# Kernel optimization log

Measured on AMD Instinct MI355X. Metric: run time of the kernel, lower is better.

The kernel has to match this reference:

```python
import jax, jax.numpy as jnp
import numpy as np

EPS = 1e-6


def setup_inputs() -> dict:
    key = jax.random.key(0)
    k1, k2 = jax.random.split(key)
    B, T = 1048576, 16
    # pred = [mean_x, mean_y, var_x, var_y]; rand keeps variances positive.
    pred = jax.random.uniform(k1, (B, 4), dtype=jnp.float32)
    true = jax.random.normal(k2, (B, T, 2), dtype=jnp.float32)
    return {"pred": pred, "true": true}


def reference(pred, true):
    # true_dist = N(tm, diag(tv)), pred_dist = N(pm, diag(pv)); loss = mean_i KL(true_i || pred_i)
    pm = pred[:, :2]                     # [B,2]
    pv = pred[:, 2:] + EPS               # [B,2]
    tm = jnp.mean(true, axis=1)          # [B,2]
    tv = jnp.var(true, axis=1, ddof=1) + EPS  # unbiased, matching torch .var()
    # Closed-form diagonal-Gaussian KL(p||q) = 0.5 * sum(log(qv/pv) + pv/qv + (qm-pm)^2/qv - 1)
    kl = 0.5 * (jnp.sum(jnp.log(pv / tv) + tv / pv + (pm - tm) ** 2 / pv, axis=-1) - 2.0)
    return jnp.mean(kl)
```

## Files before the change

### kernel.cpp

```cpp
#include <hip/hip_runtime.h>

#define KLD_EPS 1e-6f

__global__ __launch_bounds__(256) void gaze_kld_partial(
    const float* __restrict__ pred,
    const float* __restrict__ tru,
    float* __restrict__ partial,
    int B, int nTiles)
{
    __shared__ float4 lds4[2048];

    const int t    = threadIdx.x;
    const int lane = t & 63;
    const int wid  = t >> 6;

    const float4* __restrict__ tru4  = (const float4*)tru;
    const float4* __restrict__ pred4 = (const float4*)pred;

    float local = 0.0f;
    const long long totF4 = (long long)B * 8;

    for (int tb = blockIdx.x; tb < nTiles; tb += gridDim.x) {
        const long long gBase = (long long)tb * 2048;
        const int row = tb * 256 + t;

        float4 p = make_float4(0.f, 0.f, 1.f, 1.f);
        if (row < B) p = pred4[row];

        if ((tb * 256 + 256) <= B) {
            #pragma unroll
            for (int i = 0; i < 8; ++i) {
                int j   = i * 256 + wid * 64 + lane;
                int src = (j & ~7) | ((j & 7) ^ ((j >> 3) & 7));
                __builtin_amdgcn_global_load_lds(
                    (const __attribute__((address_space(1))) void*)(tru4 + gBase + src),
                    (__attribute__((address_space(3))) void*)&lds4[i * 256 + wid * 64],
                    16, 0, 0);
            }
        } else {
            #pragma unroll
            for (int i = 0; i < 8; ++i) {
                int gl = i * 256 + t;
                long long g = gBase + gl;
                float4 v = make_float4(0.f, 0.f, 0.f, 0.f);
                if (g < totF4) v = tru4[g];
                int r = gl >> 3, k = gl & 7;
                lds4[r * 8 + (k ^ (r & 7))] = v;
            }
        }

        __syncthreads();

        float sx = 0.f, sy = 0.f, sxx = 0.f, syy = 0.f;
        #pragma unroll
        for (int k = 0; k < 8; ++k) {
            float4 v = lds4[t * 8 + (k ^ (t & 7))];
            sx  += v.x + v.z;
            sy  += v.y + v.w;
            sxx += v.x * v.x + v.z * v.z;
            syy += v.y * v.y + v.w * v.w;
        }

        __syncthreads();

        if (row < B) {
            float pmx = p.x, pmy = p.y;
            float pvx = p.z + KLD_EPS, pvy = p.w + KLD_EPS;

            float tmx = sx * (1.0f / 16.0f);
            float tmy = sy * (1.0f / 16.0f);
            float tvx = (sxx - 16.0f * tmx * tmx) * (1.0f / 15.0f) + KLD_EPS;
            float tvy = (syy - 16.0f * tmy * tmy) * (1.0f / 15.0f) + KLD_EPS;

            float dx = pmx - tmx, dy = pmy - tmy;
            local += 0.5f * ( __logf(pvx / tvx) + tvx / pvx + dx * dx / pvx
                            + __logf(pvy / tvy) + tvy / pvy + dy * dy / pvy
                            - 2.0f );
        }
    }

    __shared__ float sm[4];
    #pragma unroll
    for (int off = 32; off > 0; off >>= 1)
        local += __shfl_down(local, off);
    if ((t & 63) == 0) sm[t >> 6] = local;
    __syncthreads();
    if (t == 0)
        partial[blockIdx.x] = (sm[0] + sm[1]) + (sm[2] + sm[3]);
}

__global__ __launch_bounds__(256) void gaze_kld_final(
    const float* __restrict__ partial, int n,
    float* __restrict__ out, float invB)
{
    const int t = threadIdx.x;
    float s = 0.0f;
    for (int i = t; i < n; i += blockDim.x) s += partial[i];

    __shared__ float sm[4];
    #pragma unroll
    for (int off = 32; off > 0; off >>= 1)
        s += __shfl_down(s, off);
    if ((t & 63) == 0) sm[t >> 6] = s;
    __syncthreads();
    if (t == 0)
        out[0] = ((sm[0] + sm[1]) + (sm[2] + sm[3])) * invB;
}

extern "C" void kernel_launch(void* const* d_in, const int* in_sizes, int n_in,
                              void* d_out, int out_size, void* d_ws, size_t ws_size,
                              hipStream_t stream) {
    const float* pred = (const float*)d_in[0];
    const float* tru  = (const float*)d_in[1];
    float* out = (float*)d_out;

    const int B = in_sizes[0] / 4;
    const int nTiles = (B + 255) / 256;

    int blocks = 1024;
    if (blocks > nTiles) blocks = nTiles;
    size_t maxBlocks = ws_size / sizeof(float);
    if ((size_t)blocks > maxBlocks) blocks = (int)maxBlocks;
    if (blocks < 1) blocks = 1;

    float* partials = (float*)d_ws;

    gaze_kld_partial<<<blocks, 256, 0, stream>>>(pred, tru, partials, B, nTiles);
    gaze_kld_final<<<1, 256, 0, stream>>>(partials, blocks, out, 1.0f / (float)B);
}
```

Baseline: 30.84 us.

## Fuse final reduction via atomic ticket and make LDS tiles wave-private

Each thread now reduces a row that its own wave staged through global_load_lds. The block-wide __syncthreads around the LDS tile become a per-wave vmcnt wait. The tail tile reads global memory directly instead of going through LDS. The separate final-reduction kernel is replaced by a last-block-done pattern: an atomic counter in the workspace, zeroed with hipMemsetAsync, plus a thread fence. The grid also grows from 1024 to 1280 blocks. This trades a kernel launch and block barriers for an extra memset and atomic/fence overhead, and relies on the wave-local ordering of LDS reads versus the next tile's asynchronous LDS writes.

```diff
diff --git a/kernel.cpp b/kernel.cpp
--- a/kernel.cpp
+++ b/kernel.cpp
@@ -2,13 +2,17 @@
 
 #define KLD_EPS 1e-6f
 
-__global__ __launch_bounds__(256) void gaze_kld_partial(
+__global__ __launch_bounds__(256) void gaze_kld_fused(
     const float* __restrict__ pred,
     const float* __restrict__ tru,
-    float* __restrict__ partial,
-    int B, int nTiles)
+    float* __restrict__ out,
+    float* __restrict__ partials,
+    int* __restrict__ counter,
+    int B, int nTiles, int nBlocks)
 {
     __shared__ float4 lds4[2048];
+    __shared__ float sm[4];
+    __shared__ int lastFlag;
 
     const int t    = threadIdx.x;
     const int lane = t & 63;
@@ -17,17 +21,19 @@
     const float4* __restrict__ tru4  = (const float4*)tru;
     const float4* __restrict__ pred4 = (const float4*)pred;
 
+    const int rowL = ((lane >> 3) << 5) + (wid << 3) + (lane & 7);
+    const int swz  = rowL & 7;
+
     float local = 0.0f;
-    const long long totF4 = (long long)B * 8;
 
     for (int tb = blockIdx.x; tb < nTiles; tb += gridDim.x) {
-        const long long gBase = (long long)tb * 2048;
-        const int row = tb * 256 + t;
+        const int row = tb * 256 + rowL;
+        float sx = 0.f, sy = 0.f, sxx = 0.f, syy = 0.f;
+        float4 p;
 
-        float4 p = make_float4(0.f, 0.f, 1.f, 1.f);
-        if (row < B) p = pred4[row];
-
-        if ((tb * 256 + 256) <= B) {
+        if (tb * 256 + 256 <= B) {
+            p = pred4[row];
+            const long long gBase = (long long)tb * 2048;
             #pragma unroll
             for (int i = 0; i < 8; ++i) {
                 int j   = i * 256 + wid * 64 + lane;
@@ -37,31 +43,32 @@
                     (__attribute__((address_space(3))) void*)&lds4[i * 256 + wid * 64],
                     16, 0, 0);
             }
+            asm volatile("s_waitcnt vmcnt(0)" ::: "memory");
+            __builtin_amdgcn_sched_barrier(0);
+
+            #pragma unroll
+            for (int k = 0; k < 8; ++k) {
+                float4 v = lds4[rowL * 8 + (k ^ swz)];
+                sx  += v.x + v.z;
+                sy  += v.y + v.w;
+                sxx += v.x * v.x + v.z * v.z;
+                syy += v.y * v.y + v.w * v.w;
+            }
         } else {
-            #pragma unroll
-            for (int i = 0; i < 8; ++i) {
-                int gl = i * 256 + t;
-                long long g = gBase + gl;
-                float4 v = make_float4(0.f, 0.f, 0.f, 0.f);
-                if (g < totF4) v = tru4[g];
-                int r = gl >> 3, k = gl & 7;
-                lds4[r * 8 + (k ^ (r & 7))] = v;
+            p = make_float4(0.f, 0.f, 1.f, 1.f);
+            if (row < B) {
+                p = pred4[row];
+                const float4* r4 = tru4 + (long long)row * 8;
+                #pragma unroll
+                for (int k = 0; k < 8; ++k) {
+                    float4 v = r4[k];
+                    sx  += v.x + v.z;
+                    sy  += v.y + v.w;
+                    sxx += v.x * v.x + v.z * v.z;
+                    syy += v.y * v.y + v.w * v.w;
+                }
             }
         }
-
-        __syncthreads();
-
-        float sx = 0.f, sy = 0.f, sxx = 0.f, syy = 0.f;
-        #pragma unroll
-        for (int k = 0; k < 8; ++k) {
-            float4 v = lds4[t * 8 + (k ^ (t & 7))];
-            sx  += v.x + v.z;
-            sy  += v.y + v.w;
-            sxx += v.x * v.x + v.z * v.z;
-            syy += v.y * v.y + v.w * v.w;
-        }
-
-        __syncthreads();
 
         if (row < B) {
             float pmx = p.x, pmy = p.y;
@@ -79,32 +86,33 @@
         }
     }
 
-    __shared__ float sm[4];
     #pragma unroll
     for (int off = 32; off > 0; off >>= 1)
         local += __shfl_down(local, off);
     if ((t & 63) == 0) sm[t >> 6] = local;
     __syncthreads();
-    if (t == 0)
-        partial[blockIdx.x] = (sm[0] + sm[1]) + (sm[2] + sm[3]);
-}
 
-__global__ __launch_bounds__(256) void gaze_kld_final(
-    const float* __restrict__ partial, int n,
-    float* __restrict__ out, float invB)
-{
-    const int t = threadIdx.x;
-    float s = 0.0f;
-    for (int i = t; i < n; i += blockDim.x) s += partial[i];
+    if (t == 0) {
+        partials[blockIdx.x] = (sm[0] + sm[1]) + (sm[2] + sm[3]);
+        __threadfence();
+        int ticket = atomicAdd(counter, 1);
+        lastFlag = (ticket == nBlocks - 1) ? 1 : 0;
+    }
+    __syncthreads();
 
-    __shared__ float sm[4];
-    #pragma unroll
-    for (int off = 32; off > 0; off >>= 1)
-        s += __shfl_down(s, off);
-    if ((t & 63) == 0) sm[t >> 6] = s;
-    __syncthreads();
-    if (t == 0)
-        out[0] = ((sm[0] + sm[1]) + (sm[2] + sm[3])) * invB;
+    if (lastFlag) {
+        __threadfence();
+        float s = 0.0f;
+        for (int i = t; i < nBlocks; i += 256) s += partials[i];
+        __syncthreads();
+        #pragma unroll
+        for (int off = 32; off > 0; off >>= 1)
+            s += __shfl_down(s, off);
+        if ((t & 63) == 0) sm[t >> 6] = s;
+        __syncthreads();
+        if (t == 0)
+            out[0] = ((sm[0] + sm[1]) + (sm[2] + sm[3])) * (1.0f / (float)B);
+    }
 }
 
 extern "C" void kernel_launch(void* const* d_in, const int* in_sizes, int n_in,
@@ -117,14 +125,20 @@
     const int B = in_sizes[0] / 4;
     const int nTiles = (B + 255) / 256;
 
-    int blocks = 1024;
+    int blocks = 1280;
     if (blocks > nTiles) blocks = nTiles;
-    size_t maxBlocks = ws_size / sizeof(float);
-    if ((size_t)blocks > maxBlocks) blocks = (int)maxBlocks;
+    if (ws_size >= 1024 + sizeof(float)) {
+        size_t maxBlocks = (ws_size - 1024) / sizeof(float);
+        if ((size_t)blocks > maxBlocks) blocks = (int)maxBlocks;
+    } else {
+        blocks = 1;
+    }
     if (blocks < 1) blocks = 1;
 
-    float* partials = (float*)d_ws;
+    int*   counter  = (int*)d_ws;
+    float* partials = (float*)((char*)d_ws + 1024);
 
-    gaze_kld_partial<<<blocks, 256, 0, stream>>>(pred, tru, partials, B, nTiles);
-    gaze_kld_final<<<1, 256, 0, stream>>>(partials, blocks, out, 1.0f / (float)B);
+    hipMemsetAsync(d_ws, 0, sizeof(int), stream);
+    gaze_kld_fused<<<blocks, 256, 0, stream>>>(pred, tru, out, partials, counter,
+                                               B, nTiles, blocks);
 }
```

Result: slower. 72.89 us (+136.4%).
